# Performance work log

Measured on AMD Instinct MI355X. Metric: run time of the kernel, lower is better.

The kernel has to match this reference:

```python
import jax, jax.numpy as jnp
import numpy as np

N_NODES = 32768
NUM_EDGES = 524288
NUM_GRAPHS = 32
C = 128            # hidden channels
N_LAYERS = 3       # len(hidden_channels)-1
D_IN = 144         # 4 (op embedding dim) + 140
C_MID = 80         # mem1 out
C_OUT = 64         # mem2 out / classes
H1, K1N = 5, 10    # mem1 heads / clusters
H2, K2N = 5, 1     # mem2 heads / clusters
EPS = 1e-15


def _gatv2(x, src, dst, Wl, bl, Wr, br, att, cb):
    """GATv2Conv (heads=1, negative_slope=0.2), edges src->dst incl. self loops."""
    n = x.shape[0]
    xl = x @ Wl + bl                                  # source transform [N,C]
    xr = x @ Wr + br                                  # target transform [N,C]
    e = (jax.nn.leaky_relu(xl[src] + xr[dst], 0.2) @ att)  # [E]
    m = jax.ops.segment_max(e, dst, num_segments=n)   # segment softmax over in-edges
    ee = jnp.exp(e - m[dst])
    denom = jax.ops.segment_sum(ee, dst, num_segments=n)
    alpha = ee / denom[dst]
    out = jax.ops.segment_sum(alpha[:, None] * xl[src], dst, num_segments=n)
    return out + cb


def _bn(h, gamma, beta):
    # BatchNorm1d with batch statistics (training-mode forward), eps=1e-5
    mu = h.mean(0)
    var = h.var(0)
    return (h - mu) * jax.lax.rsqrt(var + 1e-5) * gamma + beta


def _mem_pool(xd, Kmem, W):
    # xd [B,N,C], Kmem [H,K,C]; Student-t kernel, tau=1 -> (1+d)^-1
    d = (jnp.sum(xd * xd, -1)[:, :, None, None]
         + jnp.sum(Kmem * Kmem, -1)[None, None]
         - 2.0 * jnp.einsum('bnc,hkc->bnhk', xd, Kmem))  # [B,N,H,K] sq. distances
    S = 1.0 / (1.0 + d)
    S = S / S.sum(-1, keepdims=True)   # normalize over clusters
    S = S.mean(2)                      # average heads -> [B,N,K]
    out = jnp.einsum('bnk,bnc->bkc', S, xd) @ W
    return out, S


def _kl_loss(S):
    S2 = S * S / S.sum(1, keepdims=True)
    den = S2.sum(2, keepdims=True)
    den = jnp.where(S.sum(2, keepdims=True) == 0.0, 1.0, den)
    P = jnp.maximum(S2 / den, EPS)
    Sc = jnp.maximum(S, EPS)
    # KLDivLoss(reduction='batchmean'), input = log(S)
    return jnp.sum(P * (jnp.log(P) - jnp.log(Sc))) / S.shape[0]


def setup_inputs():
    key = jax.random.key(0)
    ks = jax.random.split(key, 24)
    x = jax.random.normal(ks[0], (N_NODES, D_IN), jnp.float32)
    edge_index = jax.random.randint(ks[1], (2, NUM_EDGES), 0, N_NODES, jnp.int32)
    batch = (jnp.arange(N_NODES, dtype=jnp.int32) // (N_NODES // NUM_GRAPHS))
    s = 1.0 / np.sqrt(C)
    inp = {
        'x': x, 'edge_index': edge_index, 'batch': batch,
        'W_in': jax.random.normal(ks[2], (D_IN, C), jnp.float32) / np.sqrt(D_IN),
        'b_in': jnp.zeros((C,), jnp.float32),
        'bn_gamma': jnp.ones((N_LAYERS, C), jnp.float32),
        'bn_beta': jnp.zeros((N_LAYERS, C), jnp.float32),
        'Wl': jax.random.normal(ks[3], (N_LAYERS, C, C), jnp.float32) * s,
        'bl': jnp.zeros((N_LAYERS, C), jnp.float32),
        'Wr': jax.random.normal(ks[4], (N_LAYERS, C, C), jnp.float32) * s,
        'br': jnp.zeros((N_LAYERS, C), jnp.float32),
        'att': jax.random.normal(ks[5], (N_LAYERS, C), jnp.float32) * s,
        'conv_bias': jnp.zeros((N_LAYERS, C), jnp.float32),
        'K1': jax.random.normal(ks[6], (H1, K1N, C), jnp.float32),
        'Wm1': jax.random.normal(ks[7], (C, C_MID), jnp.float32) * s,
        'K2': jax.random.normal(ks[8], (H2, K2N, C_MID), jnp.float32),
        'Wm2': jax.random.normal(ks[9], (C_MID, C_OUT), jnp.float32) / np.sqrt(C_MID),
    }
    return inp


def reference(x, edge_index, batch, W_in, b_in, bn_gamma, bn_beta,
              Wl, bl, Wr, br, att, conv_bias, K1, Wm1, K2, Wm2):
    h = x @ W_in + b_in                               # self.linear
    loops = jnp.arange(N_NODES, dtype=edge_index.dtype)
    src = jnp.concatenate([edge_index[0], loops])     # GATv2 add_self_loops=True
    dst = jnp.concatenate([edge_index[1], loops])
    for l in range(N_LAYERS):                         # DeepGCNLayer block='res+'
        t = _bn(h, bn_gamma[l], bn_beta[l])
        t = jax.nn.leaky_relu(t, 0.01)
        # dropout: identity (deterministic reference)
        t = _gatv2(t, src, dst, Wl[l], bl[l], Wr[l], br[l], att[l], conv_bias[l])
        h = h + t
    per = N_NODES // NUM_GRAPHS
    xd = h.reshape(NUM_GRAPHS, per, C)                # to_dense_batch (equal-size graphs)
    x1, S1 = _mem_pool(xd, K1, Wm1)                   # [B,10,80]
    x1 = jax.nn.leaky_relu(x1, 0.01)
    x2, S2 = _mem_pool(x1, K2, Wm2)                   # [B,1,64]
    logits = jax.nn.log_softmax(x2.squeeze(1), -1)    # [B,64]
    return logits, _kl_loss(S1) + _kl_loss(S2)
```

## Files before the change

### kernel.cpp

```cpp
#include <hip/hip_runtime.h>
#include <math.h>
#include <string.h>

#define N_NODES   32768
#define NUM_EDGES 524288
#define NUM_GRAPHS 32
#define PER_G     1024
#define C         128
#define D_IN      144
#define C_MID     80
#define C_OUT     64
#define NL        3

#define WS_H    0
#define WS_XL   16777216
#define WS_XR   33554432
#define WS_CSR  50331648
#define WS_DEG  52428800
#define WS_OFF  52559872
#define WS_CUR  52690944
#define WS_BNP  52822016
#define WS_SC   53084160
#define WS_SH   53084672
#define WS_S1   53085184
#define WS_CS   54395904
#define WS_PP   54397184
#define WS_X1   55707904
#define WS_KL   55810304

using short8 = __attribute__((ext_vector_type(8))) short;
using f32x4  = __attribute__((ext_vector_type(4))) float;

__device__ __forceinline__ float wave_sum(float v) {
  #pragma unroll
  for (int m = 1; m < 64; m <<= 1) v += __shfl_xor(v, m, 64);
  return v;
}

__device__ __forceinline__ float lrelu2(float v) { return v > 0.f ? v : 0.2f * v; }

__device__ __forceinline__ unsigned short f2bf(float f) {
  union { float f; unsigned u; } c; c.f = f;
  unsigned r = (c.u + 0x7FFFu + ((c.u >> 16) & 1u)) >> 16;
  return (unsigned short)r;
}
__device__ __forceinline__ float bflo(unsigned u) {
  union { unsigned u; float f; } c; c.u = u << 16; return c.f;
}
__device__ __forceinline__ float bfhi(unsigned u) {
  union { unsigned u; float f; } c; c.u = u & 0xFFFF0000u; return c.f;
}

__global__ void k_count(const int* __restrict__ dst, int* __restrict__ deg) {
  int e = blockIdx.x * 256 + threadIdx.x;
  if (e < NUM_EDGES) atomicAdd(&deg[dst[e]], 1);
}

__global__ __launch_bounds__(1024) void k_scan(const int* __restrict__ deg, int* __restrict__ off) {
  __shared__ int part[1024];
  int t = threadIdx.x;
  int base = t * 32;
  int s = 0;
  #pragma unroll
  for (int i = 0; i < 32; i++) s += deg[base + i];
  part[t] = s;
  __syncthreads();
  for (int d = 1; d < 1024; d <<= 1) {
    int v = (t >= d) ? part[t - d] : 0;
    __syncthreads();
    part[t] += v;
    __syncthreads();
  }
  int run = (t == 0) ? 0 : part[t - 1];
  for (int i = 0; i < 32; i++) { off[base + i] = run; run += deg[base + i]; }
}

__global__ void k_fill(const int* __restrict__ src, const int* __restrict__ dst,
                       const int* __restrict__ off, int* __restrict__ cur,
                       int* __restrict__ csr) {
  int e = blockIdx.x * 256 + threadIdx.x;
  if (e < NUM_EDGES) {
    int d = dst[e];
    int p = atomicAdd(&cur[d], 1);
    csr[off[d] + p] = src[e];
  }
}

__global__ __launch_bounds__(256) void k_lin_mfma(const float* __restrict__ x,
    const float* __restrict__ W, const float* __restrict__ bias, float* __restrict__ h) {
  __shared__ __align__(16) char smem[61440];
  char* tA = smem;
  char* tB = smem + 20480;
  int n0 = blockIdx.x * 64;
  int tid = threadIdx.x;
  for (int t = 0; t < 32; t++) {
    int cp = tid & 127;
    int node = t * 2 + (tid >> 7);
    if (cp < 80) {
      unsigned pkv = 0;
      if (cp < 72) {
        float2 xv = *(const float2*)&x[(size_t)(n0 + node) * D_IN + 2 * cp];
        pkv = ((unsigned)f2bf(xv.y) << 16) | f2bf(xv.x);
      }
      int byte = node * 320 + ((4 * cp) ^ ((node & 3) << 4));
      *(unsigned*)(tA + byte) = pkv;
    }
  }
  {
    int col = tid & 127, hh = tid >> 7;
    for (int t = 0; t < 40; t++) {
      int kp = t * 2 + hh;
      float w0 = (2 * kp < D_IN) ? W[(size_t)(2 * kp) * C + col] : 0.f;
      float w1 = (2 * kp + 1 < D_IN) ? W[(size_t)(2 * kp + 1) * C + col] : 0.f;
      unsigned pkv = ((unsigned)f2bf(w1) << 16) | f2bf(w0);
      int byte = col * 320 + ((4 * kp) ^ ((col & 3) << 4));
      *(unsigned*)(tB + byte) = pkv;
    }
  }
  __syncthreads();
  int l = tid & 63, w = tid >> 6;
  f32x4 acc[8];
  #pragma unroll
  for (int f = 0; f < 8; f++) acc[f] = (f32x4){0.f, 0.f, 0.f, 0.f};
  int arow = w * 16 + (l & 15);
  #pragma unroll
  for (int ks = 0; ks < 5; ks++) {
    int kb = ks * 64 + (l >> 4) * 16;
    short8 a = *(const short8*)(tA + arow * 320 + (kb ^ ((arow & 3) << 4)));
    #pragma unroll
    for (int f = 0; f < 8; f++) {
      int col = f * 16 + (l & 15);
      short8 b = *(const short8*)(tB + col * 320 + (kb ^ ((col & 3) << 4)));
      acc[f] = __builtin_amdgcn_mfma_f32_16x16x32_bf16(a, b, acc[f], 0, 0, 0);
    }
  }
  int rowb = n0 + w * 16 + (l >> 4) * 4;
  #pragma unroll
  for (int f = 0; f < 8; f++) {
    int col = f * 16 + (l & 15);
    float bv = bias[col];
    #pragma unroll
    for (int r = 0; r < 4; r++)
      h[(size_t)(rowb + r) * C + col] = acc[f][r] + bv;
  }
}

__global__ __launch_bounds__(128) void k_bn_part(const float* __restrict__ h, float* __restrict__ part) {
  int b = blockIdx.x; int c = threadIdx.x;
  float s = 0.f, s2 = 0.f;
  int r0 = b * 128;
  for (int r = 0; r < 128; r++) {
    float v = h[(size_t)(r0 + r) * C + c];
    s += v; s2 += v * v;
  }
  part[b * C + c] = s;
  part[256 * C + b * C + c] = s2;
}

__global__ __launch_bounds__(1024) void k_bn_fin(const float* __restrict__ part,
    const float* __restrict__ gamma, const float* __restrict__ beta,
    float* __restrict__ sc, float* __restrict__ sh) {
  __shared__ float ls[8 * 128];
  __shared__ float ls2[8 * 128];
  int c = threadIdx.x & 127, g = threadIdx.x >> 7;
  float s = 0.f, s2 = 0.f;
  for (int i = 0; i < 32; i++) {
    int b = g * 32 + i;
    s += part[b * C + c];
    s2 += part[256 * C + b * C + c];
  }
  ls[g * 128 + c] = s;
  ls2[g * 128 + c] = s2;
  __syncthreads();
  if (g == 0) {
    double S = 0.0, S2 = 0.0;
    for (int k = 0; k < 8; k++) { S += ls[k * 128 + c]; S2 += ls2[k * 128 + c]; }
    double m = S / (double)N_NODES;
    double var = S2 / (double)N_NODES - m * m;
    float rsig = (float)(1.0 / sqrt(var + 1e-5));
    float scv = rsig * gamma[c];
    sc[c] = scv;
    sh[c] = beta[c] - (float)m * scv;
  }
}

__global__ __launch_bounds__(256) void k_gemm_mfma(const float* __restrict__ h,
    const float* __restrict__ sc, const float* __restrict__ sh,
    const float* __restrict__ Wl, const float* __restrict__ bl,
    const float* __restrict__ Wr, const float* __restrict__ br,
    unsigned short* __restrict__ xl, unsigned short* __restrict__ xr) {
  __shared__ __align__(16) char smem[49152];
  char* tA = smem;
  char* tB = smem + 16384;
  int bid = blockIdx.x;
  int half = bid >> 9;
  int n0 = (bid & 511) * 64;
  const float* W = half ? Wr : Wl;
  const float* bias = half ? br : bl;
  unsigned short* out = half ? xr : xl;
  int tid = threadIdx.x;
  for (int t = 0; t < 16; t++) {
    int item = t * 256 + tid;
    int node = item >> 6;
    int cp = item & 63;
    float2 hv = *(const float2*)&h[(size_t)(n0 + node) * C + 2 * cp];
    float2 scv = *(const float2*)&sc[2 * cp];
    float2 shv = *(const float2*)&sh[2 * cp];
    float t0 = hv.x * scv.x + shv.x; t0 = t0 > 0.f ? t0 : 0.01f * t0;
    float t1 = hv.y * scv.y + shv.y; t1 = t1 > 0.f ? t1 : 0.01f * t1;
    unsigned pkv = ((unsigned)f2bf(t1) << 16) | f2bf(t0);
    int byte = node * 256 + ((4 * cp) ^ ((node & 7) << 4));
    *(unsigned*)(tA + byte) = pkv;
  }
  {
    int col = tid & 127, hh = tid >> 7;
    for (int t = 0; t < 32; t++) {
      int kp = t * 2 + hh;
      float w0 = W[(size_t)(2 * kp) * C + col];
      float w1 = W[(size_t)(2 * kp + 1) * C + col];
      unsigned pkv = ((unsigned)f2bf(w1) << 16) | f2bf(w0);
      int byte = col * 256 + ((4 * kp) ^ ((col & 7) << 4));
      *(unsigned*)(tB + byte) = pkv;
    }
  }
  __syncthreads();
  int l = tid & 63, w = tid >> 6;
  f32x4 acc[8];
  #pragma unroll
  for (int f = 0; f < 8; f++) acc[f] = (f32x4){0.f, 0.f, 0.f, 0.f};
  int arow = w * 16 + (l & 15);
  #pragma unroll
  for (int ks = 0; ks < 4; ks++) {
    int kb = ks * 64 + (l >> 4) * 16;
    short8 a = *(const short8*)(tA + arow * 256 + (kb ^ ((arow & 7) << 4)));
    #pragma unroll
    for (int f = 0; f < 8; f++) {
      int col = f * 16 + (l & 15);
      short8 b = *(const short8*)(tB + col * 256 + (kb ^ ((col & 7) << 4)));
      acc[f] = __builtin_amdgcn_mfma_f32_16x16x32_bf16(a, b, acc[f], 0, 0, 0);
    }
  }
  int rowb = n0 + w * 16 + (l >> 4) * 4;
  #pragma unroll
  for (int f = 0; f < 8; f++) {
    int col = f * 16 + (l & 15);
    float bv = bias[col];
    #pragma unroll
    for (int r = 0; r < 4; r++)
      out[(size_t)(rowb + r) * C + col] = f2bf(acc[f][r] + bv);
  }
}

#define GAT_UPD(ej, ya, yb)                                            \
  if ((ej) > m) {                                                      \
    float f_ = __expf(m - (ej));                                       \
    acc0 *= f_; acc1 *= f_; ssum *= f_; m = (ej);                      \
    ssum += 1.f; acc0 += (ya); acc1 += (yb);                           \
  } else {                                                             \
    float p_ = __expf((ej) - m);                                       \
    ssum += p_; acc0 += p_ * (ya); acc1 += p_ * (yb);                  \
  }

__global__ __launch_bounds__(64) void k_gat(float* __restrict__ h,
    const unsigned* __restrict__ xlb, const unsigned* __restrict__ xrb,
    const float* __restrict__ att, const float* __restrict__ cb,
    const int* __restrict__ off, const int* __restrict__ deg,
    const int* __restrict__ csr) {
  int d = blockIdx.x;
  int lane = threadIdx.x;
  float2 a = *(const float2*)&att[2 * lane];
  unsigned ur = xrb[d * 64 + lane];
  float xr0 = bflo(ur), xr1 = bfhi(ur);
  unsigned us = xlb[d * 64 + lane];
  float xs0 = bflo(us), xs1 = bfhi(us);
  float m = wave_sum(lrelu2(xs0 + xr0) * a.x + lrelu2(xs1 + xr1) * a.y);
  float ssum = 1.f, acc0 = xs0, acc1 = xs1;
  int o = off[d], dg = deg[d];
  int j = 0;
  for (; j + 4 <= dg; j += 4) {
    int s0 = csr[o + j + 0], s1 = csr[o + j + 1];
    int s2 = csr[o + j + 2], s3 = csr[o + j + 3];
    unsigned u0 = xlb[s0 * 64 + lane];
    unsigned u1 = xlb[s1 * 64 + lane];
    unsigned u2 = xlb[s2 * 64 + lane];
    unsigned u3 = xlb[s3 * 64 + lane];
    float y00 = bflo(u0), y01 = bfhi(u0);
    float y10 = bflo(u1), y11 = bfhi(u1);
    float y20 = bflo(u2), y21 = bfhi(u2);
    float y30 = bflo(u3), y31 = bfhi(u3);
    float t0 = lrelu2(y00 + xr0) * a.x + lrelu2(y01 + xr1) * a.y;
    float t1 = lrelu2(y10 + xr0) * a.x + lrelu2(y11 + xr1) * a.y;
    float t2 = lrelu2(y20 + xr0) * a.x + lrelu2(y21 + xr1) * a.y;
    float t3 = lrelu2(y30 + xr0) * a.x + lrelu2(y31 + xr1) * a.y;
    #pragma unroll
    for (int mm = 1; mm < 64; mm <<= 1) {
      t0 += __shfl_xor(t0, mm, 64);
      t1 += __shfl_xor(t1, mm, 64);
      t2 += __shfl_xor(t2, mm, 64);
      t3 += __shfl_xor(t3, mm, 64);
    }
    GAT_UPD(t0, y00, y01);
    GAT_UPD(t1, y10, y11);
    GAT_UPD(t2, y20, y21);
    GAT_UPD(t3, y30, y31);
  }
  for (; j < dg; j++) {
    int s = csr[o + j];
    unsigned u = xlb[s * 64 + lane];
    float y0 = bflo(u), y1 = bfhi(u);
    float ej = wave_sum(lrelu2(y0 + xr0) * a.x + lrelu2(y1 + xr1) * a.y);
    GAT_UPD(ej, y0, y1);
  }
  float inv = 1.f / ssum;
  float2 cbv = *(const float2*)&cb[2 * lane];
  float2 hv = *(float2*)&h[(size_t)d * C + 2 * lane];
  hv.x += acc0 * inv + cbv.x;
  hv.y += acc1 * inv + cbv.y;
  *(float2*)&h[(size_t)d * C + 2 * lane] = hv;
}

__global__ __launch_bounds__(320) void k_mem1(const float* __restrict__ h,
    const float* __restrict__ K1, float* __restrict__ S1, float* __restrict__ colsum) {
  __shared__ float dd[64 * 51];
  __shared__ float kn[50];
  int tid = threadIdx.x;
  int lane = tid & 63;
  int w = tid >> 6;
  int n0 = blockIdx.x * 64;
  if (tid < 50) {
    const float4* kr = reinterpret_cast<const float4*>(K1 + tid * C);
    float s = 0.f;
    for (int q = 0; q < 32; q++) {
      float4 kv = kr[q];
      s += kv.x * kv.x + kv.y * kv.y + kv.z * kv.z + kv.w * kv.w;
    }
    kn[tid] = s;
  }
  int wu = __builtin_amdgcn_readfirstlane(w);
  const float4* x4 = reinterpret_cast<const float4*>(h + (size_t)(n0 + lane) * C);
  const float4* K4 = reinterpret_cast<const float4*>(K1);
  float acc[10];
  #pragma unroll
  for (int it = 0; it < 10; it++) acc[it] = 0.f;
  float xn = 0.f;
  for (int q = 0; q < 32; q += 2) {
    float4 xa = x4[q], xb = x4[q + 1];
    xn += xa.x * xa.x + xa.y * xa.y + xa.z * xa.z + xa.w * xa.w
        + xb.x * xb.x + xb.y * xb.y + xb.z * xb.z + xb.w * xb.w;
    #pragma unroll
    for (int it = 0; it < 10; it++) {
      int j = wu + 5 * it;
      float4 ka = K4[j * 32 + q], kb = K4[j * 32 + q + 1];
      acc[it] += xa.x * ka.x + xa.y * ka.y + xa.z * ka.z + xa.w * ka.w
               + xb.x * kb.x + xb.y * kb.y + xb.z * kb.z + xb.w * kb.w;
    }
  }
  #pragma unroll
  for (int it = 0; it < 10; it++) dd[lane * 51 + wu + 5 * it] = acc[it];
  __syncthreads();
  if (tid < 64) {
    float sn[10];
    #pragma unroll
    for (int k = 0; k < 10; k++) sn[k] = 0.f;
    #pragma unroll
    for (int hd = 0; hd < 5; hd++) {
      float sh_[10]; float hs = 0.f;
      #pragma unroll
      for (int k = 0; k < 10; k++) {
        int j = hd * 10 + k;
        float dist = xn + kn[j] - 2.f * dd[tid * 51 + j];
        float s = 1.f / (1.f + dist);
        sh_[k] = s; hs += s;
      }
      float inv = 1.f / hs;
      #pragma unroll
      for (int k = 0; k < 10; k++) sn[k] += sh_[k] * inv;
    }
    int b = n0 >> 10;
    #pragma unroll
    for (int k = 0; k < 10; k++) {
      float v = 0.2f * sn[k];
      S1[(n0 + tid) * 10 + k] = v;
      float vs = wave_sum(v);
      if (tid == 0) atomicAdd(&colsum[b * 10 + k], vs);
    }
  }
}

__global__ __launch_bounds__(128) void k_pool1a(const float* __restrict__ h,
    const float* __restrict__ S1, float* __restrict__ pp) {
  int b = blockIdx.x >> 3, ch = blockIdx.x & 7;
  int c = threadIdx.x;
  float acc[10];
  #pragma unroll
  for (int k = 0; k < 10; k++) acc[k] = 0.f;
  int n0 = ch * 128;
  for (int n = 0; n < 128; n++) {
    int i = b * PER_G + n0 + n;
    float xv = h[(size_t)i * C + c];
    #pragma unroll
    for (int k = 0; k < 10; k++) acc[k] += S1[i * 10 + k] * xv;
  }
  #pragma unroll
  for (int k = 0; k < 10; k++) pp[((b * 8 + ch) * 10 + k) * C + c] = acc[k];
}

__global__ __launch_bounds__(128) void k_pool1b(const float* __restrict__ pp,
    const float* __restrict__ Wm1, float* __restrict__ x1) {
  int bk = blockIdx.x; int b = bk / 10; int k = bk - b * 10;
  int c = threadIdx.x;
  __shared__ float red[C];
  float r = 0.f;
  for (int ch = 0; ch < 8; ch++) r += pp[((b * 8 + ch) * 10 + k) * C + c];
  red[c] = r;
  __syncthreads();
  if (c < C_MID) {
    float o = 0.f;
    for (int mIdx = 0; mIdx < C; mIdx++) o += red[mIdx] * Wm1[mIdx * C_MID + c];
    o = o > 0.f ? o : 0.01f * o;
    x1[bk * C_MID + c] = o;
  }
}

__global__ __launch_bounds__(256) void k_kl1(const float* __restrict__ S1,
    const float* __restrict__ colsum, float* __restrict__ kl) {
  int i = blockIdx.x * 256 + threadIdx.x;
  int b = i >> 10;
  float s[10], q[10];
  float den = 0.f;
  #pragma unroll
  for (int k = 0; k < 10; k++) {
    s[k] = S1[i * 10 + k];
    q[k] = s[k] * s[k] / colsum[b * 10 + k];
    den += q[k];
  }
  float inv = 1.f / den;
  float term = 0.f;
  #pragma unroll
  for (int k = 0; k < 10; k++) {
    float P = fmaxf(q[k] * inv, 1e-15f);
    float Sc = fmaxf(s[k], 1e-15f);
    term += P * (logf(P) - logf(Sc));
  }
  term *= (1.f / (float)NUM_GRAPHS);
  term = wave_sum(term);
  if ((threadIdx.x & 63) == 0) atomicAdd(kl, term);
}

__global__ __launch_bounds__(128) void k_mem2(const float* __restrict__ x1,
    const float* __restrict__ Wm2, const float* __restrict__ kl, float* __restrict__ out) {
  int b = blockIdx.x;
  __shared__ float t80[C_MID];
  int tid = threadIdx.x;
  if (tid < C_MID) {
    float s = 0.f;
    #pragma unroll
    for (int k = 0; k < 10; k++) s += x1[(b * 10 + k) * C_MID + tid];
    t80[tid] = s;
  }
  __syncthreads();
  if (tid < C_OUT) {
    float o = 0.f;
    for (int mIdx = 0; mIdx < C_MID; mIdx++) o += t80[mIdx] * Wm2[mIdx * C_OUT + tid];
    float mx = o;
    #pragma unroll
    for (int d = 1; d < 64; d <<= 1) mx = fmaxf(mx, __shfl_xor(mx, d, 64));
    float p = expf(o - mx);
    float sum = p;
    #pragma unroll
    for (int d = 1; d < 64; d <<= 1) sum += __shfl_xor(sum, d, 64);
    out[b * C_OUT + tid] = o - mx - logf(sum);
  }
  if (b == 0 && tid == 127) out[NUM_GRAPHS * C_OUT] = kl[0];
}

extern "C" void kernel_launch(void* const* d_in, const int* in_sizes, int n_in,
                              void* d_out, int out_size, void* d_ws, size_t ws_size,
                              hipStream_t stream) {
  const float* x    = (const float*)d_in[0];
  const int*   ei   = (const int*)d_in[1];
  const float* W_in = (const float*)d_in[3];
  const float* b_in = (const float*)d_in[4];
  const float* bn_g = (const float*)d_in[5];
  const float* bn_b = (const float*)d_in[6];
  const float* Wl   = (const float*)d_in[7];
  const float* bl   = (const float*)d_in[8];
  const float* Wr   = (const float*)d_in[9];
  const float* br   = (const float*)d_in[10];
  const float* att  = (const float*)d_in[11];
  const float* cb   = (const float*)d_in[12];
  const float* K1   = (const float*)d_in[13];
  const float* Wm1  = (const float*)d_in[14];
  const float* Wm2  = (const float*)d_in[16];
  float* out = (float*)d_out;

  char* ws = (char*)d_ws;
  float* h    = (float*)(ws + WS_H);
  unsigned short* xlp = (unsigned short*)(ws + WS_XL);
  unsigned short* xrp = (unsigned short*)(ws + WS_XR);
  int*   csr  = (int*)(ws + WS_CSR);
  int*   deg  = (int*)(ws + WS_DEG);
  int*   off  = (int*)(ws + WS_OFF);
  int*   cur  = (int*)(ws + WS_CUR);
  float* bnp  = (float*)(ws + WS_BNP);
  float* scv  = (float*)(ws + WS_SC);
  float* shv  = (float*)(ws + WS_SH);
  float* S1p  = (float*)(ws + WS_S1);
  float* cs   = (float*)(ws + WS_CS);
  float* pp   = (float*)(ws + WS_PP);
  float* x1p  = (float*)(ws + WS_X1);
  float* klp  = (float*)(ws + WS_KL);

  const int* srcp = ei;
  const int* dstp = ei + NUM_EDGES;

  hipMemsetAsync(deg, 0, N_NODES * sizeof(int), stream);
  hipMemsetAsync(cur, 0, N_NODES * sizeof(int), stream);
  hipMemsetAsync(cs, 0, NUM_GRAPHS * 10 * sizeof(float), stream);
  hipMemsetAsync(klp, 0, sizeof(float), stream);

  k_count<<<NUM_EDGES / 256, 256, 0, stream>>>(dstp, deg);
  k_scan<<<1, 1024, 0, stream>>>(deg, off);
  k_fill<<<NUM_EDGES / 256, 256, 0, stream>>>(srcp, dstp, off, cur, csr);

  k_lin_mfma<<<N_NODES / 64, 256, 0, stream>>>(x, W_in, b_in, h);

  for (int l = 0; l < NL; l++) {
    k_bn_part<<<256, 128, 0, stream>>>(h, bnp);
    k_bn_fin<<<1, 1024, 0, stream>>>(bnp, bn_g + l * C, bn_b + l * C, scv, shv);
    k_gemm_mfma<<<2 * (N_NODES / 64), 256, 0, stream>>>(h, scv, shv,
        Wl + l * C * C, bl + l * C,
        Wr + l * C * C, br + l * C,
        xlp, xrp);
    k_gat<<<N_NODES, 64, 0, stream>>>(h, (const unsigned*)xlp, (const unsigned*)xrp,
        att + l * C, cb + l * C, off, deg, csr);
  }

  k_mem1<<<N_NODES / 64, 320, 0, stream>>>(h, K1, S1p, cs);
  k_pool1a<<<NUM_GRAPHS * 8, 128, 0, stream>>>(h, S1p, pp);
  k_pool1b<<<NUM_GRAPHS * 10, 128, 0, stream>>>(pp, Wm1, x1p);
  k_kl1<<<N_NODES / 256, 256, 0, stream>>>(S1p, cs, klp);
  k_mem2<<<NUM_GRAPHS, 128, 0, stream>>>(x1p, Wm2, klp, out);
}
```

Before: 343.8 us.

## Restructure GAT to two nodes per wave, fuse xl/xr GEMMs, widen BN and pooling grids

The GAT kernel now gives each wavefront two destination nodes, with 32 lanes handling four channels each. It uses a branchless online softmax and masks the tail edges of the shorter in-degree. The xl and xr projections are computed in one block that reuses the staged activation tile, and the BN partial-sum and pool1a kernels get finer-grained grids with a transposed partial layout for vectorized reduction. The workspace offsets are repacked to match. These changes aim to raise occupancy and cut per-node shuffle and launch overhead. The cost is idle lanes when the two paired nodes have different degrees, and more partial buffers to reduce.

```diff
diff --git a/kernel.cpp b/kernel.cpp
--- a/kernel.cpp
+++ b/kernel.cpp
@@ -1,6 +1,5 @@
 #include <hip/hip_runtime.h>
 #include <math.h>
-#include <string.h>
 
 #define N_NODES   32768
 #define NUM_EDGES 524288
@@ -14,19 +13,19 @@
 
 #define WS_H    0
 #define WS_XL   16777216
-#define WS_XR   33554432
-#define WS_CSR  50331648
-#define WS_DEG  52428800
-#define WS_OFF  52559872
-#define WS_CUR  52690944
-#define WS_BNP  52822016
-#define WS_SC   53084160
-#define WS_SH   53084672
-#define WS_S1   53085184
-#define WS_CS   54395904
-#define WS_PP   54397184
-#define WS_X1   55707904
-#define WS_KL   55810304
+#define WS_XR   25165824
+#define WS_CSR  33554432
+#define WS_DEG  35651584
+#define WS_OFF  35782656
+#define WS_CUR  35913728
+#define WS_BNP  36044800
+#define WS_SC   38141952
+#define WS_SH   38142464
+#define WS_S1   38142976
+#define WS_CS   39453696
+#define WS_PP   39454976
+#define WS_X1   44697856
+#define WS_KL   44800256
 
 using short8 = __attribute__((ext_vector_type(8))) short;
 using f32x4  = __attribute__((ext_vector_type(4))) float;
@@ -37,7 +36,7 @@
   return v;
 }
 
-__device__ __forceinline__ float lrelu2(float v) { return v > 0.f ? v : 0.2f * v; }
+__device__ __forceinline__ float lrelu2(float v) { return fmaxf(v, 0.2f * v); }
 
 __device__ __forceinline__ unsigned short f2bf(float f) {
   union { float f; unsigned u; } c; c.f = f;
@@ -148,39 +147,85 @@
 __global__ __launch_bounds__(128) void k_bn_part(const float* __restrict__ h, float* __restrict__ part) {
   int b = blockIdx.x; int c = threadIdx.x;
   float s = 0.f, s2 = 0.f;
-  int r0 = b * 128;
-  for (int r = 0; r < 128; r++) {
+  int r0 = b * 16;
+  #pragma unroll
+  for (int r = 0; r < 16; r++) {
     float v = h[(size_t)(r0 + r) * C + c];
     s += v; s2 += v * v;
   }
-  part[b * C + c] = s;
-  part[256 * C + b * C + c] = s2;
+  part[c * 2048 + b] = s;
+  part[128 * 2048 + c * 2048 + b] = s2;
 }
 
 __global__ __launch_bounds__(1024) void k_bn_fin(const float* __restrict__ part,
     const float* __restrict__ gamma, const float* __restrict__ beta,
     float* __restrict__ sc, float* __restrict__ sh) {
-  __shared__ float ls[8 * 128];
-  __shared__ float ls2[8 * 128];
-  int c = threadIdx.x & 127, g = threadIdx.x >> 7;
+  __shared__ float ls[128][8];
+  __shared__ float ls2[128][8];
+  int c = threadIdx.x >> 3, g = threadIdx.x & 7;
+  const float4* p4 = (const float4*)&part[c * 2048 + g * 256];
+  const float4* q4 = (const float4*)&part[128 * 2048 + c * 2048 + g * 256];
   float s = 0.f, s2 = 0.f;
-  for (int i = 0; i < 32; i++) {
-    int b = g * 32 + i;
-    s += part[b * C + c];
-    s2 += part[256 * C + b * C + c];
-  }
-  ls[g * 128 + c] = s;
-  ls2[g * 128 + c] = s2;
+  for (int i = 0; i < 64; i++) {
+    float4 v = p4[i];
+    s += v.x + v.y + v.z + v.w;
+    float4 u = q4[i];
+    s2 += u.x + u.y + u.z + u.w;
+  }
+  ls[c][g] = s;
+  ls2[c][g] = s2;
   __syncthreads();
   if (g == 0) {
     double S = 0.0, S2 = 0.0;
-    for (int k = 0; k < 8; k++) { S += ls[k * 128 + c]; S2 += ls2[k * 128 + c]; }
+    #pragma unroll
+    for (int k = 0; k < 8; k++) { S += ls[c][k]; S2 += ls2[c][k]; }
     double m = S / (double)N_NODES;
     double var = S2 / (double)N_NODES - m * m;
     float rsig = (float)(1.0 / sqrt(var + 1e-5));
     float scv = rsig * gamma[c];
     sc[c] = scv;
     sh[c] = beta[c] - (float)m * scv;
+  }
+}
+
+__device__ __forceinline__ void gemm_half(const char* tA, const char* tB,
+    const float* bias, unsigned short* out, int n0, int tid) {
+  int l = tid & 63, w = tid >> 6;
+  f32x4 acc[8];
+  #pragma unroll
+  for (int f = 0; f < 8; f++) acc[f] = (f32x4){0.f, 0.f, 0.f, 0.f};
+  int arow = w * 16 + (l & 15);
+  #pragma unroll
+  for (int ks = 0; ks < 4; ks++) {
+    int kb = ks * 64 + (l >> 4) * 16;
+    short8 a = *(const short8*)(tA + arow * 256 + (kb ^ ((arow & 7) << 4)));
+    #pragma unroll
+    for (int f = 0; f < 8; f++) {
+      int col = f * 16 + (l & 15);
+      short8 b = *(const short8*)(tB + col * 256 + (kb ^ ((col & 7) << 4)));
+      acc[f] = __builtin_amdgcn_mfma_f32_16x16x32_bf16(a, b, acc[f], 0, 0, 0);
+    }
+  }
+  int rowb = n0 + w * 16 + (l >> 4) * 4;
+  #pragma unroll
+  for (int f = 0; f < 8; f++) {
+    int col = f * 16 + (l & 15);
+    float bv = bias[col];
+    #pragma unroll
+    for (int r = 0; r < 4; r++)
+      out[(size_t)(rowb + r) * C + col] = f2bf(acc[f][r] + bv);
+  }
+}
+
+__device__ __forceinline__ void stage_B(char* tB, const float* __restrict__ W, int tid) {
+  int col = tid & 127, hh = tid >> 7;
+  for (int t = 0; t < 32; t++) {
+    int kp = t * 2 + hh;
+    float w0 = W[(size_t)(2 * kp) * C + col];
+    float w1 = W[(size_t)(2 * kp + 1) * C + col];
+    unsigned pkv = ((unsigned)f2bf(w1) << 16) | f2bf(w0);
+    int byte = col * 256 + ((4 * kp) ^ ((col & 7) << 4));
+    *(unsigned*)(tB + byte) = pkv;
   }
 }
 
@@ -192,12 +237,7 @@
   __shared__ __align__(16) char smem[49152];
   char* tA = smem;
   char* tB = smem + 16384;
-  int bid = blockIdx.x;
-  int half = bid >> 9;
-  int n0 = (bid & 511) * 64;
-  const float* W = half ? Wr : Wl;
-  const float* bias = half ? br : bl;
-  unsigned short* out = half ? xr : xl;
+  int n0 = blockIdx.x * 64;
   int tid = threadIdx.x;
   for (int t = 0; t < 16; t++) {
     int item = t * 256 + tid;
@@ -206,117 +246,115 @@
     float2 hv = *(const float2*)&h[(size_t)(n0 + node) * C + 2 * cp];
     float2 scv = *(const float2*)&sc[2 * cp];
     float2 shv = *(const float2*)&sh[2 * cp];
-    float t0 = hv.x * scv.x + shv.x; t0 = t0 > 0.f ? t0 : 0.01f * t0;
-    float t1 = hv.y * scv.y + shv.y; t1 = t1 > 0.f ? t1 : 0.01f * t1;
+    float t0 = hv.x * scv.x + shv.x; t0 = fmaxf(t0, 0.01f * t0);
+    float t1 = hv.y * scv.y + shv.y; t1 = fmaxf(t1, 0.01f * t1);
     unsigned pkv = ((unsigned)f2bf(t1) << 16) | f2bf(t0);
     int byte = node * 256 + ((4 * cp) ^ ((node & 7) << 4));
     *(unsigned*)(tA + byte) = pkv;
   }
-  {
-    int col = tid & 127, hh = tid >> 7;
-    for (int t = 0; t < 32; t++) {
-      int kp = t * 2 + hh;
-      float w0 = W[(size_t)(2 * kp) * C + col];
-      float w1 = W[(size_t)(2 * kp + 1) * C + col];
-      unsigned pkv = ((unsigned)f2bf(w1) << 16) | f2bf(w0);
-      int byte = col * 256 + ((4 * kp) ^ ((col & 7) << 4));
-      *(unsigned*)(tB + byte) = pkv;
-    }
-  }
-  __syncthreads();
-  int l = tid & 63, w = tid >> 6;
-  f32x4 acc[8];
-  #pragma unroll
-  for (int f = 0; f < 8; f++) acc[f] = (f32x4){0.f, 0.f, 0.f, 0.f};
-  int arow = w * 16 + (l & 15);
-  #pragma unroll
-  for (int ks = 0; ks < 4; ks++) {
-    int kb = ks * 64 + (l >> 4) * 16;
-    short8 a = *(const short8*)(tA + arow * 256 + (kb ^ ((arow & 7) << 4)));
-    #pragma unroll
-    for (int f = 0; f < 8; f++) {
-      int col = f * 16 + (l & 15);
-      short8 b = *(const short8*)(tB + col * 256 + (kb ^ ((col & 7) << 4)));
-      acc[f] = __builtin_amdgcn_mfma_f32_16x16x32_bf16(a, b, acc[f], 0, 0, 0);
-    }
-  }
-  int rowb = n0 + w * 16 + (l >> 4) * 4;
-  #pragma unroll
-  for (int f = 0; f < 8; f++) {
-    int col = f * 16 + (l & 15);
-    float bv = bias[col];
-    #pragma unroll
-    for (int r = 0; r < 4; r++)
-      out[(size_t)(rowb + r) * C + col] = f2bf(acc[f][r] + bv);
-  }
-}
-
-#define GAT_UPD(ej, ya, yb)                                            \
-  if ((ej) > m) {                                                      \
-    float f_ = __expf(m - (ej));                                       \
-    acc0 *= f_; acc1 *= f_; ssum *= f_; m = (ej);                      \
-    ssum += 1.f; acc0 += (ya); acc1 += (yb);                           \
-  } else {                                                             \
-    float p_ = __expf((ej) - m);                                       \
-    ssum += p_; acc0 += p_ * (ya); acc1 += p_ * (yb);                  \
-  }
-
-__global__ __launch_bounds__(64) void k_gat(float* __restrict__ h,
+  stage_B(tB, Wl, tid);
+  __syncthreads();
+  gemm_half(tA, tB, bl, xl, n0, tid);
+  __syncthreads();
+  stage_B(tB, Wr, tid);
+  __syncthreads();
+  gemm_half(tA, tB, br, xr, n0, tid);
+}
+
+__global__ __launch_bounds__(256) void k_gat(float* __restrict__ h,
     const unsigned* __restrict__ xlb, const unsigned* __restrict__ xrb,
     const float* __restrict__ att, const float* __restrict__ cb,
     const int* __restrict__ off, const int* __restrict__ deg,
     const int* __restrict__ csr) {
-  int d = blockIdx.x;
-  int lane = threadIdx.x;
-  float2 a = *(const float2*)&att[2 * lane];
-  unsigned ur = xrb[d * 64 + lane];
-  float xr0 = bflo(ur), xr1 = bfhi(ur);
-  unsigned us = xlb[d * 64 + lane];
-  float xs0 = bflo(us), xs1 = bfhi(us);
-  float m = wave_sum(lrelu2(xs0 + xr0) * a.x + lrelu2(xs1 + xr1) * a.y);
-  float ssum = 1.f, acc0 = xs0, acc1 = xs1;
-  int o = off[d], dg = deg[d];
-  int j = 0;
-  for (; j + 4 <= dg; j += 4) {
-    int s0 = csr[o + j + 0], s1 = csr[o + j + 1];
-    int s2 = csr[o + j + 2], s3 = csr[o + j + 3];
-    unsigned u0 = xlb[s0 * 64 + lane];
-    unsigned u1 = xlb[s1 * 64 + lane];
-    unsigned u2 = xlb[s2 * 64 + lane];
-    unsigned u3 = xlb[s3 * 64 + lane];
-    float y00 = bflo(u0), y01 = bfhi(u0);
-    float y10 = bflo(u1), y11 = bfhi(u1);
-    float y20 = bflo(u2), y21 = bfhi(u2);
-    float y30 = bflo(u3), y31 = bfhi(u3);
-    float t0 = lrelu2(y00 + xr0) * a.x + lrelu2(y01 + xr1) * a.y;
-    float t1 = lrelu2(y10 + xr0) * a.x + lrelu2(y11 + xr1) * a.y;
-    float t2 = lrelu2(y20 + xr0) * a.x + lrelu2(y21 + xr1) * a.y;
-    float t3 = lrelu2(y30 + xr0) * a.x + lrelu2(y31 + xr1) * a.y;
-    #pragma unroll
-    for (int mm = 1; mm < 64; mm <<= 1) {
+  int tid = threadIdx.x;
+  int lane = tid & 63;
+  int w = tid >> 6;
+  int half = lane >> 5;
+  int q = lane & 31;
+  int node = blockIdx.x * 8 + w * 2 + half;
+  float4 a = *(const float4*)&att[q * 4];
+  uint2 ur = *(const uint2*)&xrb[(size_t)node * 64 + q * 2];
+  float xr0 = bflo(ur.x), xr1 = bfhi(ur.x), xr2 = bflo(ur.y), xr3 = bfhi(ur.y);
+  uint2 us = *(const uint2*)&xlb[(size_t)node * 64 + q * 2];
+  float acc0 = bflo(us.x), acc1 = bfhi(us.x), acc2 = bflo(us.y), acc3 = bfhi(us.y);
+  float p0 = lrelu2(acc0 + xr0) * a.x + lrelu2(acc1 + xr1) * a.y
+           + lrelu2(acc2 + xr2) * a.z + lrelu2(acc3 + xr3) * a.w;
+  #pragma unroll
+  for (int mm = 1; mm < 32; mm <<= 1) p0 += __shfl_xor(p0, mm, 64);
+  float m = p0;
+  float ssum = 1.f;
+  int o = off[node], dg = deg[node];
+  int dgmax = max(dg, __shfl_xor(dg, 32, 64));
+  for (int j = 0; j < dgmax; j += 4) {
+    int i0 = o + ((j + 0 < dg) ? j + 0 : 0);
+    int i1 = o + ((j + 1 < dg) ? j + 1 : 0);
+    int i2 = o + ((j + 2 < dg) ? j + 2 : 0);
+    int i3 = o + ((j + 3 < dg) ? j + 3 : 0);
+    int s0 = csr[i0], s1 = csr[i1], s2 = csr[i2], s3 = csr[i3];
+    uint2 u0 = *(const uint2*)&xlb[(size_t)s0 * 64 + q * 2];
+    uint2 u1 = *(const uint2*)&xlb[(size_t)s1 * 64 + q * 2];
+    uint2 u2 = *(const uint2*)&xlb[(size_t)s2 * 64 + q * 2];
+    uint2 u3 = *(const uint2*)&xlb[(size_t)s3 * 64 + q * 2];
+    float y00 = bflo(u0.x), y01 = bfhi(u0.x), y02 = bflo(u0.y), y03 = bfhi(u0.y);
+    float y10 = bflo(u1.x), y11 = bfhi(u1.x), y12 = bflo(u1.y), y13 = bfhi(u1.y);
+    float y20 = bflo(u2.x), y21 = bfhi(u2.x), y22 = bflo(u2.y), y23 = bfhi(u2.y);
+    float y30 = bflo(u3.x), y31 = bfhi(u3.x), y32 = bflo(u3.y), y33 = bfhi(u3.y);
+    float t0 = lrelu2(y00 + xr0) * a.x + lrelu2(y01 + xr1) * a.y
+             + lrelu2(y02 + xr2) * a.z + lrelu2(y03 + xr3) * a.w;
+    float t1 = lrelu2(y10 + xr0) * a.x + lrelu2(y11 + xr1) * a.y
+             + lrelu2(y12 + xr2) * a.z + lrelu2(y13 + xr3) * a.w;
+    float t2 = lrelu2(y20 + xr0) * a.x + lrelu2(y21 + xr1) * a.y
+             + lrelu2(y22 + xr2) * a.z + lrelu2(y23 + xr3) * a.w;
+    float t3 = lrelu2(y30 + xr0) * a.x + lrelu2(y31 + xr1) * a.y
+             + lrelu2(y32 + xr2) * a.z + lrelu2(y33 + xr3) * a.w;
+    #pragma unroll
+    for (int mm = 1; mm < 32; mm <<= 1) {
       t0 += __shfl_xor(t0, mm, 64);
       t1 += __shfl_xor(t1, mm, 64);
       t2 += __shfl_xor(t2, mm, 64);
       t3 += __shfl_xor(t3, mm, 64);
     }
-    GAT_UPD(t0, y00, y01);
-    GAT_UPD(t1, y10, y11);
-    GAT_UPD(t2, y20, y21);
-    GAT_UPD(t3, y30, y31);
-  }
-  for (; j < dg; j++) {
-    int s = csr[o + j];
-    unsigned u = xlb[s * 64 + lane];
-    float y0 = bflo(u), y1 = bfhi(u);
-    float ej = wave_sum(lrelu2(y0 + xr0) * a.x + lrelu2(y1 + xr1) * a.y);
-    GAT_UPD(ej, y0, y1);
+    t0 = (j + 0 < dg) ? t0 : -1e30f;
+    t1 = (j + 1 < dg) ? t1 : -1e30f;
+    t2 = (j + 2 < dg) ? t2 : -1e30f;
+    t3 = (j + 3 < dg) ? t3 : -1e30f;
+    {
+      float nm = fmaxf(m, t0); float f = __expf(m - nm); float p = __expf(t0 - nm);
+      ssum = fmaf(ssum, f, p);
+      acc0 = fmaf(acc0, f, p * y00); acc1 = fmaf(acc1, f, p * y01);
+      acc2 = fmaf(acc2, f, p * y02); acc3 = fmaf(acc3, f, p * y03);
+      m = nm;
+    }
+    {
+      float nm = fmaxf(m, t1); float f = __expf(m - nm); float p = __expf(t1 - nm);
+      ssum = fmaf(ssum, f, p);
+      acc0 = fmaf(acc0, f, p * y10); acc1 = fmaf(acc1, f, p * y11);
+      acc2 = fmaf(acc2, f, p * y12); acc3 = fmaf(acc3, f, p * y13);
+      m = nm;
+    }
+    {
+      float nm = fmaxf(m, t2); float f = __expf(m - nm); float p = __expf(t2 - nm);
+      ssum = fmaf(ssum, f, p);
+      acc0 = fmaf(acc0, f, p * y20); acc1 = fmaf(acc1, f, p * y21);
+      acc2 = fmaf(acc2, f, p * y22); acc3 = fmaf(acc3, f, p * y23);
+      m = nm;
+    }
+    {
+      float nm = fmaxf(m, t3); float f = __expf(m - nm); float p = __expf(t3 - nm);
+      ssum = fmaf(ssum, f, p);
+      acc0 = fmaf(acc0, f, p * y30); acc1 = fmaf(acc1, f, p * y31);
+      acc2 = fmaf(acc2, f, p * y32); acc3 = fmaf(acc3, f, p * y33);
+      m = nm;
+    }
   }
   float inv = 1.f / ssum;
-  float2 cbv = *(const float2*)&cb[2 * lane];
-  float2 hv = *(float2*)&h[(size_t)d * C + 2 * lane];
+  float4 cbv = *(const float4*)&cb[q * 4];
+  float4 hv = *(float4*)&h[(size_t)node * C + q * 4];
   hv.x += acc0 * inv + cbv.x;
   hv.y += acc1 * inv + cbv.y;
-  *(float2*)&h[(size_t)d * C + 2 * lane] = hv;
+  hv.z += acc2 * inv + cbv.z;
+  hv.w += acc3 * inv + cbv.w;
+  *(float4*)&h[(size_t)node * C + q * 4] = hv;
 }
 
 __global__ __launch_bounds__(320) void k_mem1(const float* __restrict__ h,
@@ -389,20 +427,20 @@
 
 __global__ __launch_bounds__(128) void k_pool1a(const float* __restrict__ h,
     const float* __restrict__ S1, float* __restrict__ pp) {
-  int b = blockIdx.x >> 3, ch = blockIdx.x & 7;
+  int b = blockIdx.x >> 5, ch = blockIdx.x & 31;
   int c = threadIdx.x;
   float acc[10];
   #pragma unroll
   for (int k = 0; k < 10; k++) acc[k] = 0.f;
-  int n0 = ch * 128;
-  for (int n = 0; n < 128; n++) {
+  int n0 = ch * 32;
+  for (int n = 0; n < 32; n++) {
     int i = b * PER_G + n0 + n;
     float xv = h[(size_t)i * C + c];
     #pragma unroll
     for (int k = 0; k < 10; k++) acc[k] += S1[i * 10 + k] * xv;
   }
   #pragma unroll
-  for (int k = 0; k < 10; k++) pp[((b * 8 + ch) * 10 + k) * C + c] = acc[k];
+  for (int k = 0; k < 10; k++) pp[(size_t)((b * 32 + ch) * 10 + k) * C + c] = acc[k];
 }
 
 __global__ __launch_bounds__(128) void k_pool1b(const float* __restrict__ pp,
@@ -411,13 +449,13 @@
   int c = threadIdx.x;
   __shared__ float red[C];
   float r = 0.f;
-  for (int ch = 0; ch < 8; ch++) r += pp[((b * 8 + ch) * 10 + k) * C + c];
+  for (int ch = 0; ch < 32; ch++) r += pp[(size_t)((b * 32 + ch) * 10 + k) * C + c];
   red[c] = r;
   __syncthreads();
   if (c < C_MID) {
     float o = 0.f;
     for (int mIdx = 0; mIdx < C; mIdx++) o += red[mIdx] * Wm1[mIdx * C_MID + c];
-    o = o > 0.f ? o : 0.01f * o;
+    o = fmaxf(o, 0.01f * o);
     x1[bk * C_MID + c] = o;
   }
 }
@@ -526,18 +564,18 @@
   k_lin_mfma<<<N_NODES / 64, 256, 0, stream>>>(x, W_in, b_in, h);
 
   for (int l = 0; l < NL; l++) {
-    k_bn_part<<<256, 128, 0, stream>>>(h, bnp);
+    k_bn_part<<<2048, 128, 0, stream>>>(h, bnp);
     k_bn_fin<<<1, 1024, 0, stream>>>(bnp, bn_g + l * C, bn_b + l * C, scv, shv);
-    k_gemm_mfma<<<2 * (N_NODES / 64), 256, 0, stream>>>(h, scv, shv,
+    k_gemm_mfma<<<N_NODES / 64, 256, 0, stream>>>(h, scv, shv,
         Wl + l * C * C, bl + l * C,
         Wr + l * C * C, br + l * C,
         xlp, xrp);
-    k_gat<<<N_NODES, 64, 0, stream>>>(h, (const unsigned*)xlp, (const unsigned*)xrp,
+    k_gat<<<N_NODES / 8, 256, 0, stream>>>(h, (const unsigned*)xlp, (const unsigned*)xrp,
         att + l * C, cb + l * C, off, deg, csr);
   }
 
   k_mem1<<<N_NODES / 64, 320, 0, stream>>>(h, K1, S1p, cs);
-  k_pool1a<<<NUM_GRAPHS * 8, 128, 0, stream>>>(h, S1p, pp);
+  k_pool1a<<<NUM_GRAPHS * 32, 128, 0, stream>>>(h, S1p, pp);
   k_pool1b<<<NUM_GRAPHS * 10, 128, 0, stream>>>(pp, Wm1, x1p);
   k_kl1<<<N_NODES / 256, 256, 0, stream>>>(S1p, cs, klp);
   k_mem2<<<NUM_GRAPHS, 128, 0, stream>>>(x1p, Wm2, klp, out);
```

Measured after the change: 506.4 us. +47.3%, slower.
